# Optimization experiments

Measured on AMD Instinct MI355X. Metric: run time of the kernel, lower is better.

The kernel has to match this reference:

```python
import jax, jax.numpy as jnp
import numpy as np

EPS = 1e-5
KERNELS = [3, 3, 5, 7]  # 2*i+1 for i>=1, first layer k=3


def _conv_relu_bn(x, w, b, gamma, beta, rmean, rvar):
    # x: [B, Cin, S], w: [Cout, Cin, K]
    k = w.shape[-1]
    y = jax.lax.conv_general_dilated(
        x, w, window_strides=(1,), padding=[(k // 2, k // 2)],
        dimension_numbers=("NCW", "OIW", "NCW"))
    y = y + b[None, :, None]
    y = jax.nn.relu(y)
    # BatchNorm1d in inference mode (running stats)
    inv = gamma[None, :, None] / jnp.sqrt(rvar[None, :, None] + EPS)
    return (y - rmean[None, :, None]) * inv + beta[None, :, None]


def setup_inputs() -> dict:
    key = jax.random.key(0)
    ks = jax.random.split(key, 32)
    B, S = 128, 8192
    inp = {"x": jax.random.normal(ks[0], (B, 4, S), dtype=jnp.float32)}
    cin = 4
    for i, k in enumerate(KERNELS):
        inp[f"w{i}"] = jax.random.normal(ks[1 + i], (32, cin, k), dtype=jnp.float32) * 0.1
        inp[f"b{i}"] = jnp.zeros((32,), jnp.float32)
        inp[f"g{i}"] = jnp.ones((32,), jnp.float32)   # BN gamma
        inp[f"bb{i}"] = jnp.zeros((32,), jnp.float32)  # BN beta
        inp[f"rm{i}"] = jnp.zeros((32,), jnp.float32)  # running mean
        inp[f"rv{i}"] = jnp.ones((32,), jnp.float32)   # running var
        cin = 32
    inp["fw1"] = jax.random.normal(ks[10], (16, 32), dtype=jnp.float32) * 0.1
    inp["fb1"] = jnp.zeros((16,), jnp.float32)
    inp["fw2"] = jax.random.normal(ks[11], (1, 16), dtype=jnp.float32) * 0.1
    inp["fb2"] = jnp.zeros((1,), jnp.float32)
    return inp


def reference(x,
              w0, b0, g0, bb0, rm0, rv0,
              w1, b1, g1, bb1, rm1, rv1,
              w2, b2, g2, bb2, rm2, rv2,
              w3, b3, g3, bb3, rm3, rv3,
              fw1, fb1, fw2, fb2):
    x = _conv_relu_bn(x, w0, b0, g0, bb0, rm0, rv0)
    x = _conv_relu_bn(x, w1, b1, g1, bb1, rm1, rv1)
    x = _conv_relu_bn(x, w2, b2, g2, bb2, rm2, rv2)
    x = _conv_relu_bn(x, w3, b3, g3, bb3, rm3, rv3)
    # [B, 32, S] -> [B, S, 32]; the original per-timestep MLP loop is one batched GEMM
    h = jnp.einsum("bcs,hc->bsh", x, fw1) + fb1
    h = jax.nn.relu(h)  # Dropout(0.1) is identity in eval
    out = jnp.einsum("bsh,oh->bso", h, fw2) + fb2
    return out[..., 0]  # squeeze(-1) -> [B, S]
```

## Files before the change

### kernel.cpp

```cpp
#include <hip/hip_runtime.h>

#define SEQ    8192
#define S_TILE 180
#define NROW   198
#define CS     1608
#define NTHR   256
#define NREC   33
#define BN_HALFOFF (NREC*512)

typedef __attribute__((ext_vector_type(8))) _Float16 half8;
typedef __attribute__((ext_vector_type(4))) _Float16 half4v;
typedef __attribute__((ext_vector_type(4))) float    f32x4;

__device__ __forceinline__ int uni(int v){ return __builtin_amdgcn_readfirstlane(v); }

template<int K>
__device__ __forceinline__ float fold_bias(const float* __restrict__ W, int co,
    const float* __restrict__ gp, const float* __restrict__ bbp,
    const float* __restrict__ rmp, const float* __restrict__ rvp)
{
    float acc = 0.f;
#pragma unroll
    for (int ci = 0; ci < 32; ++ci) {
        float sp = gp[ci] * rsqrtf(rvp[ci] + 1e-5f);
        float tp = bbp[ci] - rmp[ci]*sp;
        float wsum = 0.f;
#pragma unroll
        for (int tap = 0; tap < K; ++tap) wsum += W[(co*32 + ci)*K + tap];
        acc += wsum * tp;
    }
    return acc;
}

extern "C" __global__ void prep_kernel(
    const float* w0, const float* w1, const float* w2, const float* w3,
    const float* b0, const float* g0, const float* bb0, const float* rm0, const float* rv0,
    const float* b1, const float* g1, const float* bb1, const float* rm1, const float* rv1,
    const float* b2, const float* g2, const float* bb2, const float* rm2, const float* rv2,
    const float* b3, const float* g3, const float* bb3, const float* rm3, const float* rv3,
    const float* fw1, const float* fb1, _Float16* ws)
{
    const int tid = threadIdx.x;
    const int rec = blockIdx.x;
    if (rec < NREC) {
        if (tid < 64) {
            const int lane = tid;
            half8 h;
            if (rec < 2) {
                int co = rec*16 + (lane & 15);
#pragma unroll
                for (int j = 0; j < 8; ++j) {
                    int k = (lane >> 4)*8 + j;
                    float wv = (k < 12) ? w0[(co*4 + (k & 3))*3 + (k >> 2)] : 0.0f;
                    h[j] = (_Float16)wv;
                }
            } else {
                const float* W; const float *gp, *rvp; int K, r2;
                if      (rec < 8)  { W = w1;  K = 3; r2 = rec - 2;  gp = g0; rvp = rv0; }
                else if (rec < 18) { W = w2;  K = 5; r2 = rec - 8;  gp = g1; rvp = rv1; }
                else if (rec < 32) { W = w3;  K = 7; r2 = rec - 18; gp = g2; rvp = rv2; }
                else               { W = fw1; K = 1; r2 = 0;        gp = g3; rvp = rv3; }
                int tap = r2 >> 1, mh = r2 & 1;
                int co  = mh*16 + (lane & 15);
                int ci0 = (lane >> 4) * 8;
#pragma unroll
                for (int j = 0; j < 8; ++j) {
                    int ci = ci0 + j;
                    float wv = W[(co*32 + ci)*K + tap];
                    wv *= gp[ci] * rsqrtf(rvp[ci] + 1e-5f);
                    h[j] = (_Float16)wv;
                }
            }
            *(half8*)(ws + rec*512 + lane*8) = h;
        }
    } else {
        float* fa = (float*)(ws + BN_HALFOFF);
        if (tid < 128) {
            int l = tid >> 5, co = tid & 31;
            const float *g, *bb, *rm, *rv, *bi;
            if      (l == 0) { g=g0; bb=bb0; rm=rm0; rv=rv0; bi=b0; }
            else if (l == 1) { g=g1; bb=bb1; rm=rm1; rv=rv1; bi=b1; }
            else if (l == 2) { g=g2; bb=bb2; rm=rm2; rv=rv2; bi=b2; }
            else             { g=g3; bb=bb3; rm=rm3; rv=rv3; bi=b3; }
            float s = g[co] * rsqrtf(rv[co] + 1e-5f);
            float t = bb[co] - rm[co]*s;
            float bias = bi[co];
            if      (l == 1) bias += fold_bias<3>(w1, co, g0, bb0, rm0, rv0);
            else if (l == 2) bias += fold_bias<5>(w2, co, g1, bb1, rm1, rv1);
            else if (l == 3) bias += fold_bias<7>(w3, co, g2, bb2, rm2, rv2);
            fa[(l*32 + co)*2 + 0] = bias;
            fa[(l*32 + co)*2 + 1] = -t / s;
        } else if (tid < 144) {
            int hh = tid - 128;
            float acc = fb1[hh];
#pragma unroll
            for (int c = 0; c < 32; ++c) {
                float s3 = g3[c] * rsqrtf(rv3[c] + 1e-5f);
                float t3 = bb3[c] - rm3[c]*s3;
                acc += fw1[hh*32 + c] * t3;
            }
            fa[256 + hh] = acc;
        }
    }
}

__device__ __forceinline__ void conv_epi(
    const f32x4 (*acc)[2], const float2* __restrict__ bo,
    _Float16* outb, int s0, int doff, int ntb, int q, int n)
{
#pragma unroll
    for (int nt = 0; nt < 3; ++nt) {
        int pos = (ntb + nt)*16 + n;
        bool oob = (unsigned)(s0 + doff + pos) >= SEQ;
#pragma unroll
        for (int mh = 0; mh < 2; ++mh) {
            int co0 = mh*16 + q*4;
            half4v hv;
#pragma unroll
            for (int r = 0; r < 4; ++r) {
                float2 p = bo[co0 + r];
                float v = fmaxf(acc[nt][mh][r] + p.x, 0.0f);
                if (oob) v = p.y;
                hv[r] = (_Float16)v;
            }
            int cb = mh*2 + (q >> 1);
            *(half4v*)(outb + cb*CS + pos*8 + (q & 1)*4) = hv;
        }
    }
}

template<int K, int DOFF>
__device__ __forceinline__ void conv_layer(
    const _Float16* __restrict__ rec, const float2* __restrict__ bo,
    const _Float16* in, _Float16* outb, int s0, int ntb, int lane)
{
    const int q = lane >> 4, n = lane & 15;
    const _Float16* bbase = in + q*CS + (ntb*16 + n)*8;

    f32x4 acc[3][2];
#pragma unroll
    for (int nt = 0; nt < 3; ++nt)
#pragma unroll
        for (int mh = 0; mh < 2; ++mh) acc[nt][mh] = (f32x4){0.f, 0.f, 0.f, 0.f};

    half8 a0 = *(const half8*)(rec + 0*512 + lane*8);
    half8 a1 = *(const half8*)(rec + 1*512 + lane*8);
    half8 b0 = *(const half8*)(bbase + 0*128);
    half8 b1 = *(const half8*)(bbase + 1*128);
    half8 b2 = *(const half8*)(bbase + 2*128);

#pragma unroll
    for (int tap = 0; tap < K; ++tap) {
        half8 na0, na1, nb0, nb1, nb2;
        if (tap + 1 < K) {
            na0 = *(const half8*)(rec + ((tap+1)*2 + 0)*512 + lane*8);
            na1 = *(const half8*)(rec + ((tap+1)*2 + 1)*512 + lane*8);
            nb0 = *(const half8*)(bbase + 0*128 + (tap+1)*8);
            nb1 = *(const half8*)(bbase + 1*128 + (tap+1)*8);
            nb2 = *(const half8*)(bbase + 2*128 + (tap+1)*8);
        }
        acc[0][0] = __builtin_amdgcn_mfma_f32_16x16x32_f16(a0, b0, acc[0][0], 0, 0, 0);
        acc[0][1] = __builtin_amdgcn_mfma_f32_16x16x32_f16(a1, b0, acc[0][1], 0, 0, 0);
        acc[1][0] = __builtin_amdgcn_mfma_f32_16x16x32_f16(a0, b1, acc[1][0], 0, 0, 0);
        acc[1][1] = __builtin_amdgcn_mfma_f32_16x16x32_f16(a1, b1, acc[1][1], 0, 0, 0);
        acc[2][0] = __builtin_amdgcn_mfma_f32_16x16x32_f16(a0, b2, acc[2][0], 0, 0, 0);
        acc[2][1] = __builtin_amdgcn_mfma_f32_16x16x32_f16(a1, b2, acc[2][1], 0, 0, 0);
        if (tap + 1 < K) { a0 = na0; a1 = na1; b0 = nb0; b1 = nb1; b2 = nb2; }
    }
    conv_epi(acc, bo, outb, s0, DOFF, ntb, q, n);
}

__device__ __forceinline__ void conv_layer0(
    const _Float16* __restrict__ rec, const float2* __restrict__ bo,
    const _Float16* in, _Float16* outb, int s0, int ntb, int lane)
{
    const int q = lane >> 4, n = lane & 15;
    const _Float16* bbase = in + (q & 1)*CS + (ntb*16 + n)*8;

    half8 a0 = *(const half8*)(rec + 0*512 + lane*8);
    half8 a1 = *(const half8*)(rec + 1*512 + lane*8);

    f32x4 acc[3][2];
#pragma unroll
    for (int nt = 0; nt < 3; ++nt)
#pragma unroll
        for (int mh = 0; mh < 2; ++mh) acc[nt][mh] = (f32x4){0.f, 0.f, 0.f, 0.f};

#pragma unroll
    for (int nt = 0; nt < 3; ++nt) {
        half8 bf = *(const half8*)(bbase + nt*128);
        acc[nt][0] = __builtin_amdgcn_mfma_f32_16x16x32_f16(a0, bf, acc[nt][0], 0, 0, 0);
        acc[nt][1] = __builtin_amdgcn_mfma_f32_16x16x32_f16(a1, bf, acc[nt][1], 0, 0, 0);
    }
    conv_epi(acc, bo, outb, s0, -6, ntb, q, n);
}

extern "C" __global__ void __launch_bounds__(NTHR, 6)
dnashape_mfma(const float* __restrict__ x, const _Float16* __restrict__ ws,
              const float* __restrict__ fw2, const float* __restrict__ fb2,
              float* __restrict__ out)
{
    __shared__ _Float16 bufA[4*CS];
    __shared__ _Float16 bufB[4*CS];

    const int tid  = threadIdx.x;
    const int tile = blockIdx.x;
    const int s0   = tile * S_TILE;
    const int b    = blockIdx.y;

    {
        const float* xb = x + b*4*SEQ;
        for (int li = tid; li < NROW; li += NTHR) {
            _Float16 h[16];
#pragma unroll
            for (int tap = 0; tap < 3; ++tap) {
                int sg = s0 - 7 + li + tap;
                bool ok = (unsigned)sg < SEQ;
#pragma unroll
                for (int ci = 0; ci < 4; ++ci)
                    h[tap*4 + ci] = (_Float16)(ok ? xb[ci*SEQ + sg] : 0.f);
            }
#pragma unroll
            for (int j = 12; j < 16; ++j) h[j] = (_Float16)0.f;
            *(half8*)(&bufB[0*CS + li*8]) = *(half8*)(h);
            *(half8*)(&bufB[1*CS + li*8]) = *(half8*)(h + 8);
        }
        if (tid < 32) {
            const half8 z8 = {0,0,0,0,0,0,0,0};
            *(half8*)(&bufA[(tid >> 3)*CS + (192 + (tid & 7))*8]) = z8;
        }
    }
    __syncthreads();

    const int lane = tid & 63;
    const int wv   = uni(tid >> 6);
    const int ntb  = wv * 3;
    const float*  fa = (const float*)(ws + BN_HALFOFF);
    const float2* bo = (const float2*)fa;

    conv_layer0             (ws,           bo,      bufB, bufA, s0, ntb, lane);
    __syncthreads();
    conv_layer<3, -5>(ws +  2*512,   bo + 32, bufA, bufB, s0, ntb, lane);
    __syncthreads();
    conv_layer<5, -3>(ws +  8*512,   bo + 64, bufB, bufA, s0, ntb, lane);
    __syncthreads();
    conv_layer<7,  0>(ws + 18*512,   bo + 96, bufA, bufB, s0, ntb, lane);
    __syncthreads();

    {
        const int q = lane >> 4, n = lane & 15;
        half8 am = *(const half8*)(ws + 32*512 + lane*8);
        float fb1v[4], fw2v[4];
#pragma unroll
        for (int r = 0; r < 4; ++r) { fb1v[r] = fa[256 + q*4 + r]; fw2v[r] = fw2[q*4 + r]; }
        float fb2v = fb2[0];
#pragma unroll
        for (int nt = 0; nt < 3; ++nt) {
            int pos = (ntb + nt)*16 + n;
            half8 bf = *(const half8*)(&bufB[q*CS + pos*8]);
            f32x4 d = {0.f, 0.f, 0.f, 0.f};
            d = __builtin_amdgcn_mfma_f32_16x16x32_f16(am, bf, d, 0, 0, 0);
            float part = 0.f;
#pragma unroll
            for (int r = 0; r < 4; ++r) part += fmaxf(d[r] + fb1v[r], 0.f)*fw2v[r];
            part += __shfl_xor(part, 16, 64);
            part += __shfl_xor(part, 32, 64);
            if (lane < 16) {
                int g = s0 + pos;
                if (pos < S_TILE && g < SEQ) out[b*SEQ + g] = part + fb2v;
            }
        }
    }
}

extern "C" void kernel_launch(void* const* d_in, const int* in_sizes, int n_in,
                              void* d_out, int out_size, void* d_ws, size_t ws_size,
                              hipStream_t stream) {
    const float* p[29];
    for (int i = 0; i < 29; ++i) p[i] = (const float*)d_in[i];
    _Float16* ws = (_Float16*)d_ws;

    prep_kernel<<<dim3(NREC + 1), 144, 0, stream>>>(
        p[1], p[7], p[13], p[19],
        p[2], p[3], p[4], p[5], p[6],
        p[8], p[9], p[10], p[11], p[12],
        p[14], p[15], p[16], p[17], p[18],
        p[20], p[21], p[22], p[23], p[24],
        p[25], p[26], ws);

    dim3 grid((SEQ + S_TILE - 1) / S_TILE, 128);
    dnashape_mfma<<<grid, NTHR, 0, stream>>>(p[0], (const _Float16*)ws,
                                             p[27], p[28], (float*)d_out);
}
```

Before: 173.3 us.

## Keep last conv layer in registers and feed MLP directly, permuting channel order

```diff
diff --git a/kernel.cpp b/kernel.cpp
--- a/kernel.cpp
+++ b/kernel.cpp
@@ -9,7 +9,6 @@
 #define BN_HALFOFF (NREC*512)
 
 typedef __attribute__((ext_vector_type(8))) _Float16 half8;
-typedef __attribute__((ext_vector_type(4))) _Float16 half4v;
 typedef __attribute__((ext_vector_type(4))) float    f32x4;
 
 __device__ __forceinline__ int uni(int v){ return __builtin_amdgcn_readfirstlane(v); }
@@ -45,12 +44,13 @@
     if (rec < NREC) {
         if (tid < 64) {
             const int lane = tid;
+            const int q = lane >> 4;
             half8 h;
             if (rec < 2) {
                 int co = rec*16 + (lane & 15);
 #pragma unroll
                 for (int j = 0; j < 8; ++j) {
-                    int k = (lane >> 4)*8 + j;
+                    int k = q*8 + j;
                     float wv = (k < 12) ? w0[(co*4 + (k & 3))*3 + (k >> 2)] : 0.0f;
                     h[j] = (_Float16)wv;
                 }
@@ -62,10 +62,9 @@
                 else               { W = fw1; K = 1; r2 = 0;        gp = g3; rvp = rv3; }
                 int tap = r2 >> 1, mh = r2 & 1;
                 int co  = mh*16 + (lane & 15);
-                int ci0 = (lane >> 4) * 8;
 #pragma unroll
                 for (int j = 0; j < 8; ++j) {
-                    int ci = ci0 + j;
+                    int ci = ((j >> 2) << 4) + q*4 + (j & 3);
                     float wv = W[(co*32 + ci)*K + tap];
                     wv *= gp[ci] * rsqrtf(rvp[ci] + 1e-5f);
                     h[j] = (_Float16)wv;
@@ -104,31 +103,6 @@
     }
 }
 
-__device__ __forceinline__ void conv_epi(
-    const f32x4 (*acc)[2], const float2* __restrict__ bo,
-    _Float16* outb, int s0, int doff, int ntb, int q, int n)
-{
-#pragma unroll
-    for (int nt = 0; nt < 3; ++nt) {
-        int pos = (ntb + nt)*16 + n;
-        bool oob = (unsigned)(s0 + doff + pos) >= SEQ;
-#pragma unroll
-        for (int mh = 0; mh < 2; ++mh) {
-            int co0 = mh*16 + q*4;
-            half4v hv;
-#pragma unroll
-            for (int r = 0; r < 4; ++r) {
-                float2 p = bo[co0 + r];
-                float v = fmaxf(acc[nt][mh][r] + p.x, 0.0f);
-                if (oob) v = p.y;
-                hv[r] = (_Float16)v;
-            }
-            int cb = mh*2 + (q >> 1);
-            *(half4v*)(outb + cb*CS + pos*8 + (q & 1)*4) = hv;
-        }
-    }
-}
-
 template<int K, int DOFF>
 __device__ __forceinline__ void conv_layer(
     const _Float16* __restrict__ rec, const float2* __restrict__ bo,
@@ -137,37 +111,49 @@
     const int q = lane >> 4, n = lane & 15;
     const _Float16* bbase = in + q*CS + (ntb*16 + n)*8;
 
+    float oobc[8];
     f32x4 acc[3][2];
-#pragma unroll
-    for (int nt = 0; nt < 3; ++nt)
-#pragma unroll
-        for (int mh = 0; mh < 2; ++mh) acc[nt][mh] = (f32x4){0.f, 0.f, 0.f, 0.f};
-
-    half8 a0 = *(const half8*)(rec + 0*512 + lane*8);
-    half8 a1 = *(const half8*)(rec + 1*512 + lane*8);
-    half8 b0 = *(const half8*)(bbase + 0*128);
-    half8 b1 = *(const half8*)(bbase + 1*128);
-    half8 b2 = *(const half8*)(bbase + 2*128);
+    {
+        float bias[8];
+#pragma unroll
+        for (int i = 0; i < 8; ++i) {
+            float2 p = bo[(i >> 2)*16 + q*4 + (i & 3)];
+            bias[i] = p.x; oobc[i] = p.y;
+        }
+#pragma unroll
+        for (int nt = 0; nt < 3; ++nt)
+#pragma unroll
+            for (int mh = 0; mh < 2; ++mh)
+                acc[nt][mh] = (f32x4){bias[mh*4+0], bias[mh*4+1], bias[mh*4+2], bias[mh*4+3]};
+    }
 
 #pragma unroll
     for (int tap = 0; tap < K; ++tap) {
-        half8 na0, na1, nb0, nb1, nb2;
-        if (tap + 1 < K) {
-            na0 = *(const half8*)(rec + ((tap+1)*2 + 0)*512 + lane*8);
-            na1 = *(const half8*)(rec + ((tap+1)*2 + 1)*512 + lane*8);
-            nb0 = *(const half8*)(bbase + 0*128 + (tap+1)*8);
-            nb1 = *(const half8*)(bbase + 1*128 + (tap+1)*8);
-            nb2 = *(const half8*)(bbase + 2*128 + (tap+1)*8);
-        }
-        acc[0][0] = __builtin_amdgcn_mfma_f32_16x16x32_f16(a0, b0, acc[0][0], 0, 0, 0);
-        acc[0][1] = __builtin_amdgcn_mfma_f32_16x16x32_f16(a1, b0, acc[0][1], 0, 0, 0);
-        acc[1][0] = __builtin_amdgcn_mfma_f32_16x16x32_f16(a0, b1, acc[1][0], 0, 0, 0);
-        acc[1][1] = __builtin_amdgcn_mfma_f32_16x16x32_f16(a1, b1, acc[1][1], 0, 0, 0);
-        acc[2][0] = __builtin_amdgcn_mfma_f32_16x16x32_f16(a0, b2, acc[2][0], 0, 0, 0);
-        acc[2][1] = __builtin_amdgcn_mfma_f32_16x16x32_f16(a1, b2, acc[2][1], 0, 0, 0);
-        if (tap + 1 < K) { a0 = na0; a1 = na1; b0 = nb0; b1 = nb1; b2 = nb2; }
-    }
-    conv_epi(acc, bo, outb, s0, DOFF, ntb, q, n);
+        half8 a0 = *(const half8*)(rec + (tap*2 + 0)*512 + lane*8);
+        half8 a1 = *(const half8*)(rec + (tap*2 + 1)*512 + lane*8);
+#pragma unroll
+        for (int nt = 0; nt < 3; ++nt) {
+            half8 bf = *(const half8*)(bbase + nt*128 + tap*8);
+            acc[nt][0] = __builtin_amdgcn_mfma_f32_16x16x32_f16(a0, bf, acc[nt][0], 0, 0, 0);
+            acc[nt][1] = __builtin_amdgcn_mfma_f32_16x16x32_f16(a1, bf, acc[nt][1], 0, 0, 0);
+        }
+    }
+
+#pragma unroll
+    for (int nt = 0; nt < 3; ++nt) {
+        int pos = (ntb + nt)*16 + n;
+        bool oob = (unsigned)(s0 + DOFF + pos) >= SEQ;
+        half8 hv;
+#pragma unroll
+        for (int mh = 0; mh < 2; ++mh)
+#pragma unroll
+            for (int r = 0; r < 4; ++r) {
+                float v = fmaxf(acc[nt][mh][r], 0.0f);
+                if (oob) v = oobc[mh*4 + r];
+                hv[mh*4 + r] = (_Float16)v;
+            }
+        *(half8*)(outb + q*CS + pos*8) = hv;
+    }
 }
 
 __device__ __forceinline__ void conv_layer0(
@@ -177,22 +163,46 @@
     const int q = lane >> 4, n = lane & 15;
     const _Float16* bbase = in + (q & 1)*CS + (ntb*16 + n)*8;
 
+    float oobc[8];
+    f32x4 acc[3][2];
+    {
+        float bias[8];
+#pragma unroll
+        for (int i = 0; i < 8; ++i) {
+            float2 p = bo[(i >> 2)*16 + q*4 + (i & 3)];
+            bias[i] = p.x; oobc[i] = p.y;
+        }
+#pragma unroll
+        for (int nt = 0; nt < 3; ++nt)
+#pragma unroll
+            for (int mh = 0; mh < 2; ++mh)
+                acc[nt][mh] = (f32x4){bias[mh*4+0], bias[mh*4+1], bias[mh*4+2], bias[mh*4+3]};
+    }
+
     half8 a0 = *(const half8*)(rec + 0*512 + lane*8);
     half8 a1 = *(const half8*)(rec + 1*512 + lane*8);
-
-    f32x4 acc[3][2];
-#pragma unroll
-    for (int nt = 0; nt < 3; ++nt)
-#pragma unroll
-        for (int mh = 0; mh < 2; ++mh) acc[nt][mh] = (f32x4){0.f, 0.f, 0.f, 0.f};
-
 #pragma unroll
     for (int nt = 0; nt < 3; ++nt) {
         half8 bf = *(const half8*)(bbase + nt*128);
         acc[nt][0] = __builtin_amdgcn_mfma_f32_16x16x32_f16(a0, bf, acc[nt][0], 0, 0, 0);
         acc[nt][1] = __builtin_amdgcn_mfma_f32_16x16x32_f16(a1, bf, acc[nt][1], 0, 0, 0);
     }
-    conv_epi(acc, bo, outb, s0, -6, ntb, q, n);
+
+#pragma unroll
+    for (int nt = 0; nt < 3; ++nt) {
+        int pos = (ntb + nt)*16 + n;
+        bool oob = (unsigned)(s0 - 6 + pos) >= SEQ;
+        half8 hv;
+#pragma unroll
+        for (int mh = 0; mh < 2; ++mh)
+#pragma unroll
+            for (int r = 0; r < 4; ++r) {
+                float v = fmaxf(acc[nt][mh][r], 0.0f);
+                if (oob) v = oobc[mh*4 + r];
+                hv[mh*4 + r] = (_Float16)v;
+            }
+        *(half8*)(outb + q*CS + pos*8) = hv;
+    }
 }
 
 extern "C" __global__ void __launch_bounds__(NTHR, 6)
@@ -238,28 +248,61 @@
     const float*  fa = (const float*)(ws + BN_HALFOFF);
     const float2* bo = (const float2*)fa;
 
-    conv_layer0             (ws,           bo,      bufB, bufA, s0, ntb, lane);
+    conv_layer0      (ws,          bo,      bufB, bufA, s0, ntb, lane);
     __syncthreads();
-    conv_layer<3, -5>(ws +  2*512,   bo + 32, bufA, bufB, s0, ntb, lane);
+    conv_layer<3, -5>(ws +  2*512, bo + 32, bufA, bufB, s0, ntb, lane);
     __syncthreads();
-    conv_layer<5, -3>(ws +  8*512,   bo + 64, bufB, bufA, s0, ntb, lane);
-    __syncthreads();
-    conv_layer<7,  0>(ws + 18*512,   bo + 96, bufA, bufB, s0, ntb, lane);
+    conv_layer<5, -3>(ws +  8*512, bo + 64, bufB, bufA, s0, ntb, lane);
     __syncthreads();
 
     {
         const int q = lane >> 4, n = lane & 15;
+        const _Float16* rec3 = ws + 18*512;
+        const _Float16* bbase = bufA + q*CS + (ntb*16 + n)*8;
+        const float2* bo3 = bo + 96;
+
+        f32x4 acc[3][2];
+        {
+            float bias[8];
+#pragma unroll
+            for (int i = 0; i < 8; ++i)
+                bias[i] = bo3[(i >> 2)*16 + q*4 + (i & 3)].x;
+#pragma unroll
+            for (int nt = 0; nt < 3; ++nt)
+#pragma unroll
+                for (int mh = 0; mh < 2; ++mh)
+                    acc[nt][mh] = (f32x4){bias[mh*4+0], bias[mh*4+1], bias[mh*4+2], bias[mh*4+3]};
+        }
+
+#pragma unroll
+        for (int tap = 0; tap < 7; ++tap) {
+            half8 a0 = *(const half8*)(rec3 + (tap*2 + 0)*512 + lane*8);
+            half8 a1 = *(const half8*)(rec3 + (tap*2 + 1)*512 + lane*8);
+#pragma unroll
+            for (int nt = 0; nt < 3; ++nt) {
+                half8 bf = *(const half8*)(bbase + nt*128 + tap*8);
+                acc[nt][0] = __builtin_amdgcn_mfma_f32_16x16x32_f16(a0, bf, acc[nt][0], 0, 0, 0);
+                acc[nt][1] = __builtin_amdgcn_mfma_f32_16x16x32_f16(a1, bf, acc[nt][1], 0, 0, 0);
+            }
+        }
+
         half8 am = *(const half8*)(ws + 32*512 + lane*8);
         float fb1v[4], fw2v[4];
 #pragma unroll
         for (int r = 0; r < 4; ++r) { fb1v[r] = fa[256 + q*4 + r]; fw2v[r] = fw2[q*4 + r]; }
         float fb2v = fb2[0];
+
 #pragma unroll
         for (int nt = 0; nt < 3; ++nt) {
             int pos = (ntb + nt)*16 + n;
-            half8 bf = *(const half8*)(&bufB[q*CS + pos*8]);
+            half8 hv;
+#pragma unroll
+            for (int mh = 0; mh < 2; ++mh)
+#pragma unroll
+                for (int r = 0; r < 4; ++r)
+                    hv[mh*4 + r] = (_Float16)fmaxf(acc[nt][mh][r], 0.0f);
             f32x4 d = {0.f, 0.f, 0.f, 0.f};
-            d = __builtin_amdgcn_mfma_f32_16x16x32_f16(am, bf, d, 0, 0, 0);
+            d = __builtin_amdgcn_mfma_f32_16x16x32_f16(am, hv, d, 0, 0, 0);
             float part = 0.f;
 #pragma unroll
             for (int r = 0; r < 4; ++r) part += fmaxf(d[r] + fb1v[r], 0.f)*fw2v[r];
```

After: 171.4 us (median of 2 runs). Within noise of the previous version (-1.1%).
